# Kernel optimization log

Measured on AMD Instinct MI355X. Metric: run time of the kernel, lower is better.

Reference implementation:

```python
import jax, jax.numpy as jnp
import numpy as np

D_MODEL = 1024
N_HEADS = 16
D_K = D_MODEL // N_HEADS
B, L = 2, 2048


def setup_inputs() -> dict:
    key = jax.random.key(0)
    ks = jax.random.split(key, 13)
    s = 0.02
    inp = {
        'query': jax.random.normal(ks[0], (B, L, D_MODEL), jnp.float32),
        'key': jax.random.normal(ks[1], (B, L, D_MODEL), jnp.float32),
        'value': jax.random.normal(ks[2], (B, L, D_MODEL), jnp.float32),
        'mask': jax.random.randint(ks[3], (1, 1, L, L), 0, 2).astype(bool),
        'W_q': jax.random.normal(ks[4], (D_MODEL, D_MODEL), jnp.float32) * s,
        'b_q': jnp.zeros((D_MODEL,), jnp.float32),
        'W_k': jax.random.normal(ks[5], (D_MODEL, D_MODEL), jnp.float32) * s,
        'b_k': jnp.zeros((D_MODEL,), jnp.float32),
        'W_v': jax.random.normal(ks[6], (D_MODEL, D_MODEL), jnp.float32) * s,
        'b_v': jnp.zeros((D_MODEL,), jnp.float32),
        'W_o': jax.random.normal(ks[7], (D_MODEL, D_MODEL), jnp.float32) * s,
        'b_o': jnp.zeros((D_MODEL,), jnp.float32),
    }
    return inp


def _split_heads(x):
    b, l, _ = x.shape
    return x.reshape(b, l, N_HEADS, D_K).transpose(0, 2, 1, 3)  # [B,H,L,dk]


def reference(query, key, value, mask, W_q, b_q, W_k, b_k, W_v, b_v, W_o, b_o):
    q = _split_heads(query @ W_q + b_q)
    k = _split_heads(key @ W_k + b_k)
    v = _split_heads(value @ W_v + b_v)
    # Unscaled attention logits [B,H,L,L] (NO 1/sqrt(dk))
    logits = jnp.einsum('bhqd,bhkd->bhqk', q, k)
    logits = jnp.where(mask, -jnp.inf, logits)
    w = jax.nn.softmax(logits, axis=-1)
    w = jnp.nan_to_num(w, nan=0.0)  # fully-masked rows -> zeros
    attended = jnp.einsum('bhqk,bhkd->bhqd', w, v)
    # dropout in eval mode = identity; combine heads
    out = attended.transpose(0, 2, 1, 3).reshape(B, L, D_MODEL)
    return out @ W_o + b_o
```

## Files before the change

kernel.cpp:

```cpp
#include <hip/hip_runtime.h>
#include <hip/hip_bf16.h>
#include <stdint.h>


typedef __bf16 bf16;
typedef __bf16 bf16x8 __attribute__((ext_vector_type(8)));
typedef float f32x4 __attribute__((ext_vector_type(4)));

#define AS1 __attribute__((address_space(1)))
#define AS3 __attribute__((address_space(3)))

__device__ __forceinline__ void g2l16(const void* g, void* l) {
    __builtin_amdgcn_global_load_lds((AS1 void*)g, (AS3 void*)l, 16, 0, 0);
}

__device__ __forceinline__ bool lane_masked(unsigned long long m) {
#if __has_builtin(__builtin_amdgcn_inverse_ballot_w64)
    return __builtin_amdgcn_inverse_ballot_w64(m);
#else
    return (m >> (threadIdx.x & 63)) & 1ull;
#endif
}

#define LOG2E 1.44269504088896f

__global__ __launch_bounds__(256) void cvt3_kernel(const float* __restrict__ a0,
                                                   const float* __restrict__ a1,
                                                   const float* __restrict__ a2,
                                                   bf16* o0, bf16* o1, bf16* o2) {
    int y = blockIdx.y;
    const float* in = (y == 0) ? a0 : (y == 1) ? a1 : a2;
    bf16* out = (y == 0) ? o0 : (y == 1) ? o1 : o2;
    int idx = blockIdx.x * 256 + threadIdx.x;
    float4 v = ((const float4*)in)[idx];
    __align__(8) bf16 o[4];
    o[0] = (bf16)v.x; o[1] = (bf16)v.y; o[2] = (bf16)v.z; o[3] = (bf16)v.w;
    *(uint2*)(out + (size_t)idx * 4) = *(const uint2*)o;
}

__global__ __launch_bounds__(256) void mdetect_kernel(const unsigned int* __restrict__ w,
                                                      int* __restrict__ flag) {
    int idx = blockIdx.x * 256 + threadIdx.x;
    unsigned v = w[idx];
    int f = 0;
    if (v == 0x3F800000u) f = 2;
    else if (v > 1u) f = 1;
    unsigned long long b1 = __ballot(f & 1);
    unsigned long long b2 = __ballot(f & 2);
    if ((threadIdx.x & 63) == 0) {
        int agg = (b1 ? 1 : 0) | (b2 ? 2 : 0);
        if (agg) atomicOr(flag, agg);
    }
}

__global__ __launch_bounds__(256) void mpack_kernel(const void* __restrict__ mask,
                                                    unsigned long long* __restrict__ mb,
                                                    const int* __restrict__ flag) {
    int idx = blockIdx.x * 256 + threadIdx.x;
    int f = *flag;
    bool v;
    if (f & 2)      v = ((const float*)mask)[idx] != 0.0f;
    else if (f & 1) v = ((const unsigned char*)mask)[idx] != 0;
    else            v = ((const int*)mask)[idx] != 0;
    unsigned long long b = __ballot(v);
    if ((threadIdx.x & 63) == 0) mb[idx >> 6] = b;
}

__global__ __launch_bounds__(256) void rpack_kernel(const unsigned long long* __restrict__ mb,
                                                    unsigned long long* __restrict__ rmb) {
    int task = blockIdx.x * 4 + (threadIdx.x >> 6);
    int qg = task >> 5, kt = task & 31;
    int lane = threadIdx.x & 63, quad = lane >> 4, col = lane & 15;
    #pragma unroll
    for (int r = 0; r < 4; ++r) {
        unsigned long long wrow = mb[(size_t)(qg * 16 + quad * 4 + r) * 32 + kt];
        #pragma unroll
        for (int nt = 0; nt < 4; ++nt) {
            unsigned long long b = __ballot(((wrow >> (nt * 16 + col)) & 1ull) != 0);
            if (lane == 0) rmb[(size_t)task * 16 + r * 4 + nt] = b;
        }
    }
}

__global__ __launch_bounds__(256) void wtrans_kernel(const float* W0, const float* W1,
                                                     const float* W2, const float* W3,
                                                     bf16* T0, bf16* T1, bf16* T2, bf16* T3) {
    const float* W; bf16* T;
    int y = blockIdx.y;
    if (y == 0)      { W = W0; T = T0; }
    else if (y == 1) { W = W1; T = T1; }
    else if (y == 2) { W = W2; T = T2; }
    else             { W = W3; T = T3; }
    int tx = blockIdx.x & 15, ty = blockIdx.x >> 4;
    int n0 = tx * 64, k0 = ty * 64;
    __shared__ __align__(16) bf16 t[64 * 72];
    int tid = threadIdx.x;
    #pragma unroll
    for (int rr = 0; rr < 4; ++rr) {
        int idx = rr * 256 + tid;
        int r = idx >> 4, c4 = (idx & 15) * 4;
        float4 v = *(const float4*)(W + (size_t)(k0 + r) * 1024 + n0 + c4);
        __align__(8) bf16 o[4];
        o[0] = (bf16)v.x; o[1] = (bf16)v.y; o[2] = (bf16)v.z; o[3] = (bf16)v.w;
        *(uint2*)&t[r * 72 + c4] = *(const uint2*)o;
    }
    __syncthreads();
    #pragma unroll
    for (int rr = 0; rr < 2; ++rr) {
        int idx = rr * 256 + tid;
        int n = idx >> 3, kc = (idx & 7) * 8;
        __align__(16) bf16 o[8];
        #pragma unroll
        for (int j = 0; j < 8; ++j) o[j] = t[(kc + j) * 72 + n];
        *(uint4*)(T + (size_t)(n0 + n) * 1024 + k0 + kc) = *(const uint4*)o;
    }
}

template <int MODE>
__device__ __forceinline__ void gemm128_core(const bf16* __restrict__ A,
                                             const bf16* __restrict__ Bt,
                                             const float* __restrict__ bias,
                                             void* __restrict__ Out, int bm, int bn,
                                             float scale) {
    __shared__ __align__(16) bf16 la[128 * 32];
    __shared__ __align__(16) bf16 lb[128 * 32];
    int tid = threadIdx.x;
    int w = tid >> 6, lane = tid & 63;
    int quad = lane >> 4, col = lane & 15;
    int wm = w >> 1, wn = w & 1;
    int m0 = bm * 128, n0 = bn * 128;
    f32x4 acc[4][4];
    f32x4 z = {0.f, 0.f, 0.f, 0.f};
    #pragma unroll
    for (int i = 0; i < 4; ++i)
        #pragma unroll
        for (int j = 0; j < 4; ++j) acc[i][j] = z;
    int srow = lane >> 2;
    int skc = (lane & 3) * 8;
    for (int kt = 0; kt < 32; ++kt) {
        int kk = kt * 32;
        __syncthreads();
        #pragma unroll
        for (int rr = 0; rr < 2; ++rr) {
            int ch = rr * 4 + w;
            int row = ch * 16 + srow;
            g2l16(A + (size_t)(m0 + row) * 1024 + kk + skc, &la[ch * 512]);
            g2l16(Bt + (size_t)(n0 + row) * 1024 + kk + skc, &lb[ch * 512]);
        }
        __syncthreads();
        bf16x8 af[4], bfr[4];
        #pragma unroll
        for (int mt = 0; mt < 4; ++mt)
            af[mt] = *(const bf16x8*)&la[(wm * 64 + mt * 16 + col) * 32 + quad * 8];
        #pragma unroll
        for (int nt = 0; nt < 4; ++nt)
            bfr[nt] = *(const bf16x8*)&lb[(wn * 64 + nt * 16 + col) * 32 + quad * 8];
        #pragma unroll
        for (int mt = 0; mt < 4; ++mt)
            #pragma unroll
            for (int nt = 0; nt < 4; ++nt)
                acc[mt][nt] = __builtin_amdgcn_mfma_f32_16x16x32_bf16(
                    af[mt], bfr[nt], acc[mt][nt], 0, 0, 0);
    }
    float bia[4];
    #pragma unroll
    for (int nt = 0; nt < 4; ++nt) bia[nt] = bias[n0 + wn * 64 + nt * 16 + col];
    #pragma unroll
    for (int mt = 0; mt < 4; ++mt) {
        #pragma unroll
        for (int nt = 0; nt < 4; ++nt) {
            #pragma unroll
            for (int r = 0; r < 4; ++r) {
                int m = m0 + wm * 64 + mt * 16 + quad * 4 + r;
                int n = n0 + wn * 64 + nt * 16 + col;
                float v = (acc[mt][nt][r] + bia[nt]) * scale;
                if (MODE == 0) {
                    int b = m >> 11, l = m & 2047, h = n >> 6, d = n & 63;
                    ((bf16*)Out)[(((size_t)b * 16 + h) * 2048 + l) * 64 + d] = (bf16)v;
                } else {
                    int b = m >> 11, l = m & 2047, h = n >> 6, d = n & 63;
                    ((bf16*)Out)[(((size_t)b * 16 + h) * 64 + d) * 2048 + l] = (bf16)v;
                }
            }
        }
    }
}

__global__ __launch_bounds__(256) void qkv_kernel(
    const bf16* Xq, const bf16* Xk, const bf16* Xv,
    const bf16* Wq, const bf16* Wk, const bf16* Wv,
    const float* bq, const float* bk, const float* bv,
    bf16* Qh, bf16* Kh, bf16* Vt) {
    int y = blockIdx.y;
    int bm = blockIdx.x >> 3, bn = blockIdx.x & 7;
    if (y == 0)      gemm128_core<0>(Xq, Wq, bq, Qh, bm, bn, LOG2E);
    else if (y == 1) gemm128_core<0>(Xk, Wk, bk, Kh, bm, bn, 1.0f);
    else             gemm128_core<2>(Xv, Wv, bv, Vt, bm, bn, 1.0f);
}

__global__ __launch_bounds__(256) void ogemm_kernel(const bf16* __restrict__ A,
                                                    const bf16* __restrict__ Wt,
                                                    const float* __restrict__ bias,
                                                    float* __restrict__ Out) {
    int bm = blockIdx.x >> 3, bn = blockIdx.x & 7;
    __shared__ __align__(16) bf16 la[64 * 32];
    __shared__ __align__(16) bf16 lb[128 * 32];
    int tid = threadIdx.x;
    int w = tid >> 6, lane = tid & 63;
    int quad = lane >> 4, col = lane & 15;
    int m0 = bm * 64, n0 = bn * 128;
    f32x4 acc[4][2];
    f32x4 z = {0.f, 0.f, 0.f, 0.f};
    #pragma unroll
    for (int i = 0; i < 4; ++i) { acc[i][0] = z; acc[i][1] = z; }
    int srow = lane >> 2;
    int skc = (lane & 3) * 8;
    for (int kt = 0; kt < 32; ++kt) {
        int kk = kt * 32;
        __syncthreads();
        g2l16(A + (size_t)(m0 + w * 16 + srow) * 1024 + kk + skc, &la[w * 512]);
        #pragma unroll
        for (int rr = 0; rr < 2; ++rr) {
            int ch = rr * 4 + w;
            g2l16(Wt + (size_t)(n0 + ch * 16 + srow) * 1024 + kk + skc, &lb[ch * 512]);
        }
        __syncthreads();
        bf16x8 af[4], bfr[2];
        #pragma unroll
        for (int mt = 0; mt < 4; ++mt)
            af[mt] = *(const bf16x8*)&la[(mt * 16 + col) * 32 + quad * 8];
        #pragma unroll
        for (int nt = 0; nt < 2; ++nt)
            bfr[nt] = *(const bf16x8*)&lb[(w * 32 + nt * 16 + col) * 32 + quad * 8];
        #pragma unroll
        for (int mt = 0; mt < 4; ++mt)
            #pragma unroll
            for (int nt = 0; nt < 2; ++nt)
                acc[mt][nt] = __builtin_amdgcn_mfma_f32_16x16x32_bf16(
                    af[mt], bfr[nt], acc[mt][nt], 0, 0, 0);
    }
    float bia[2];
    bia[0] = bias[n0 + w * 32 + col];
    bia[1] = bias[n0 + w * 32 + 16 + col];
    #pragma unroll
    for (int mt = 0; mt < 4; ++mt)
        #pragma unroll
        for (int nt = 0; nt < 2; ++nt)
            #pragma unroll
            for (int r = 0; r < 4; ++r)
                Out[(size_t)(m0 + mt * 16 + quad * 4 + r) * 1024 +
                    n0 + w * 32 + nt * 16 + col] = acc[mt][nt][r] + bia[nt];
}

__global__ __launch_bounds__(128) void attn_kernel(const bf16* __restrict__ Qh,
                                                   const bf16* __restrict__ Kh,
                                                   const bf16* __restrict__ Vt,
                                                   const unsigned long long* __restrict__ rmb,
                                                   bf16* __restrict__ att) {
    int bh = blockIdx.x, qt = blockIdx.y;
    int b = bh >> 4, h = bh & 15;
    int q0 = qt * 64;
    __shared__ __align__(16) bf16 ks[64 * 64];
    __shared__ __align__(16) bf16 vs[64 * 64];
    __shared__ __align__(16) bf16 ps[2 * 32 * 72];
    int tid = threadIdx.x;
    int w = tid >> 6, lane = tid & 63;
    int quad = lane >> 4, col = lane & 15;
    int c7 = col & 7;
    int sr = lane >> 3;
    int sg = (lane & 7) ^ sr;
    int swz0 = (quad ^ c7) * 8;
    int swz1 = ((4 + quad) ^ c7) * 8;

    int mofs = __builtin_amdgcn_readfirstlane((qt * 4 + w * 2) * 512);

    #pragma unroll
    for (int i = 0; i < 4; ++i) {
        int ch = w * 4 + i;
        g2l16(Qh + ((size_t)bh * 2048 + q0 + ch * 8 + sr) * 64 + sg * 8, &ks[ch * 512]);
    }
    __syncthreads();
    bf16x8 aq[2][2];
    #pragma unroll
    for (int mt = 0; mt < 2; ++mt) {
        aq[mt][0] = *(const bf16x8*)&ks[(w * 32 + mt * 16 + col) * 64 + swz0];
        aq[mt][1] = *(const bf16x8*)&ks[(w * 32 + mt * 16 + col) * 64 + swz1];
    }
    bf16x8 onesf;
    #pragma unroll
    for (int i = 0; i < 8; ++i) onesf[i] = (bf16)1.0f;

    f32x4 z = {0.f, 0.f, 0.f, 0.f};
    f32x4 O[2][4], R[2];
    #pragma unroll
    for (int mt = 0; mt < 2; ++mt) {
        R[mt] = z;
        #pragma unroll
        for (int i = 0; i < 4; ++i) O[mt][i] = z;
    }

    for (int kt = 0; kt < 32; ++kt) {
        __syncthreads();
        #pragma unroll
        for (int i = 0; i < 4; ++i) {
            int ch = w * 4 + i;
            int r = ch * 8 + sr;
            g2l16(Kh + ((size_t)bh * 2048 + kt * 64 + r) * 64 + sg * 8, &ks[ch * 512]);
            g2l16(Vt + ((size_t)bh * 64 + r) * 2048 + kt * 64 + sg * 8, &vs[ch * 512]);
        }
        __syncthreads();

        f32x4 s[2][4];
        #pragma unroll
        for (int nt = 0; nt < 4; ++nt) {
            s[0][nt] = z; s[1][nt] = z;
            bf16x8 bk0 = *(const bf16x8*)&ks[(nt * 16 + col) * 64 + swz0];
            s[0][nt] = __builtin_amdgcn_mfma_f32_16x16x32_bf16(aq[0][0], bk0, s[0][nt], 0, 0, 0);
            s[1][nt] = __builtin_amdgcn_mfma_f32_16x16x32_bf16(aq[1][0], bk0, s[1][nt], 0, 0, 0);
            bf16x8 bk1 = *(const bf16x8*)&ks[(nt * 16 + col) * 64 + swz1];
            s[0][nt] = __builtin_amdgcn_mfma_f32_16x16x32_bf16(aq[0][1], bk1, s[0][nt], 0, 0, 0);
            s[1][nt] = __builtin_amdgcn_mfma_f32_16x16x32_bf16(aq[1][1], bk1, s[1][nt], 0, 0, 0);
        }

        #pragma unroll
        for (int mt = 0; mt < 2; ++mt) {
            const unsigned long long* mw = rmb + mofs + mt * 512 + kt * 16;
            #pragma unroll
            for (int r = 0; r < 4; ++r) {
                #pragma unroll
                for (int nt = 0; nt < 4; ++nt) {
                    float p = __builtin_amdgcn_exp2f(s[mt][nt][r]);
                    if (lane_masked(mw[r * 4 + nt])) p = 0.0f;
                    ps[w * 2304 + (mt * 16 + quad * 4 + r) * 72 + nt * 16 + col] = (bf16)p;
                }
            }
        }

        bf16x8 ap[2][2];
        #pragma unroll
        for (int mt = 0; mt < 2; ++mt) {
            ap[mt][0] = *(const bf16x8*)&ps[w * 2304 + (mt * 16 + col) * 72 + quad * 8];
            ap[mt][1] = *(const bf16x8*)&ps[w * 2304 + (mt * 16 + col) * 72 + 32 + quad * 8];
        }
        #pragma unroll
        for (int dt = 0; dt < 4; ++dt) {
            bf16x8 bv0 = *(const bf16x8*)&vs[(dt * 16 + col) * 64 + swz0];
            O[0][dt] = __builtin_amdgcn_mfma_f32_16x16x32_bf16(ap[0][0], bv0, O[0][dt], 0, 0, 0);
            O[1][dt] = __builtin_amdgcn_mfma_f32_16x16x32_bf16(ap[1][0], bv0, O[1][dt], 0, 0, 0);
            bf16x8 bv1 = *(const bf16x8*)&vs[(dt * 16 + col) * 64 + swz1];
            O[0][dt] = __builtin_amdgcn_mfma_f32_16x16x32_bf16(ap[0][1], bv1, O[0][dt], 0, 0, 0);
            O[1][dt] = __builtin_amdgcn_mfma_f32_16x16x32_bf16(ap[1][1], bv1, O[1][dt], 0, 0, 0);
        }
        #pragma unroll
        for (int mt = 0; mt < 2; ++mt) {
            R[mt] = __builtin_amdgcn_mfma_f32_16x16x32_bf16(ap[mt][0], onesf, R[mt], 0, 0, 0);
            R[mt] = __builtin_amdgcn_mfma_f32_16x16x32_bf16(ap[mt][1], onesf, R[mt], 0, 0, 0);
        }
    }

    #pragma unroll
    for (int mt = 0; mt < 2; ++mt) {
        #pragma unroll
        for (int r = 0; r < 4; ++r) {
            float rsv = R[mt][r];
            float inv = (rsv > 0.f) ? 1.0f / rsv : 0.f;
            int qg = q0 + w * 32 + mt * 16 + quad * 4 + r;
            #pragma unroll
            for (int dt = 0; dt < 4; ++dt) {
                float ov = O[mt][dt][r] * inv;
                att[((size_t)b * 2048 + qg) * 1024 + h * 64 + dt * 16 + col] = (bf16)ov;
            }
        }
    }
}

extern "C" void kernel_launch(void* const* d_in, const int* in_sizes, int n_in,
                              void* d_out, int out_size, void* d_ws, size_t ws_size,
                              hipStream_t stream) {
    (void)in_sizes; (void)n_in; (void)out_size; (void)ws_size;
    const float* query = (const float*)d_in[0];
    const float* key_  = (const float*)d_in[1];
    const float* value = (const float*)d_in[2];
    const void*  mask  = d_in[3];
    const float* W_q = (const float*)d_in[4];
    const float* b_q = (const float*)d_in[5];
    const float* W_k = (const float*)d_in[6];
    const float* b_k = (const float*)d_in[7];
    const float* W_v = (const float*)d_in[8];
    const float* b_v = (const float*)d_in[9];
    const float* W_o = (const float*)d_in[10];
    const float* b_o = (const float*)d_in[11];

    char* ws = (char*)d_ws;
    bf16* Xq  = (bf16*)(ws + 0);
    bf16* Xk  = (bf16*)(ws + 8388608);
    bf16* Xv  = (bf16*)(ws + 16777216);
    bf16* Wtq = (bf16*)(ws + 25165824);
    bf16* Wtk = (bf16*)(ws + 27262976);
    bf16* Wtv = (bf16*)(ws + 29360128);
    bf16* Wto = (bf16*)(ws + 31457280);
    bf16* Qh  = (bf16*)(ws + 33554432);
    bf16* Kh  = (bf16*)(ws + 41943040);
    bf16* Vt  = (bf16*)(ws + 50331648);
    bf16* att = (bf16*)(ws + 58720256);
    unsigned long long* mb  = (unsigned long long*)(ws + 67108864);
    unsigned long long* rmb = (unsigned long long*)(ws + 67633152);
    int* flag = (int*)(ws + 68157440);

    hipMemsetAsync(flag, 0, 4, stream);
    mdetect_kernel<<<4096, 256, 0, stream>>>((const unsigned int*)mask, flag);
    mpack_kernel<<<16384, 256, 0, stream>>>(mask, mb, flag);
    rpack_kernel<<<1024, 256, 0, stream>>>(mb, rmb);

    cvt3_kernel<<<dim3(4096, 3), 256, 0, stream>>>(query, key_, value, Xq, Xk, Xv);
    wtrans_kernel<<<dim3(256, 4), 256, 0, stream>>>(W_q, W_k, W_v, W_o, Wtq, Wtk, Wtv, Wto);

    qkv_kernel<<<dim3(256, 3), 256, 0, stream>>>(Xq, Xk, Xv, Wtq, Wtk, Wtv,
                                                 b_q, b_k, b_v, Qh, Kh, Vt);
    attn_kernel<<<dim3(32, 32), 128, 0, stream>>>(Qh, Kh, Vt, rmb, att);
    ogemm_kernel<<<512, 256, 0, stream>>>(att, Wto, b_o, (float*)d_out);
}
```

Baseline: 271.8 us.

## Fuse activation fp32->bf16 conversion into QKV GEMM and merge mask prep kernels

Removes the separate cvt3 kernel so the QKV GEMM loads fp32 activations directly, converts them in registers and stores bf16 into LDS. The mask detect/pack/repack chain becomes a single-wavefront detect kernel that samples only the first 4096 words, plus a packing path folded into the weight-transpose kernel. This cuts several launches and the intermediate bf16 and bitmask buffers. In exchange, A-tile loads in the GEMM become synchronous register loads instead of global_load_lds. The mask-type detection now looks at a sample rather than the whole mask, which could misclassify some masks.

```diff
diff --git a/kernel.cpp b/kernel.cpp
--- a/kernel.cpp
+++ b/kernel.cpp
@@ -24,69 +24,50 @@
 
 #define LOG2E 1.44269504088896f
 
-__global__ __launch_bounds__(256) void cvt3_kernel(const float* __restrict__ a0,
-                                                   const float* __restrict__ a1,
-                                                   const float* __restrict__ a2,
-                                                   bf16* o0, bf16* o1, bf16* o2) {
-    int y = blockIdx.y;
-    const float* in = (y == 0) ? a0 : (y == 1) ? a1 : a2;
-    bf16* out = (y == 0) ? o0 : (y == 1) ? o1 : o2;
-    int idx = blockIdx.x * 256 + threadIdx.x;
-    float4 v = ((const float4*)in)[idx];
-    __align__(8) bf16 o[4];
-    o[0] = (bf16)v.x; o[1] = (bf16)v.y; o[2] = (bf16)v.z; o[3] = (bf16)v.w;
-    *(uint2*)(out + (size_t)idx * 4) = *(const uint2*)o;
-}
-
-__global__ __launch_bounds__(256) void mdetect_kernel(const unsigned int* __restrict__ w,
-                                                      int* __restrict__ flag) {
-    int idx = blockIdx.x * 256 + threadIdx.x;
-    unsigned v = w[idx];
+__global__ __launch_bounds__(64) void mdetect_kernel(const unsigned int* __restrict__ w,
+                                                     int* __restrict__ flag) {
+    int lane = threadIdx.x;
     int f = 0;
-    if (v == 0x3F800000u) f = 2;
-    else if (v > 1u) f = 1;
+    #pragma unroll
+    for (int i = 0; i < 64; ++i) {
+        unsigned v = w[i * 64 + lane];
+        if (v == 0x3F800000u) f |= 2;
+        else if (v > 1u) f |= 1;
+    }
     unsigned long long b1 = __ballot(f & 1);
     unsigned long long b2 = __ballot(f & 2);
-    if ((threadIdx.x & 63) == 0) {
-        int agg = (b1 ? 1 : 0) | (b2 ? 2 : 0);
-        if (agg) atomicOr(flag, agg);
-    }
-}
-
-__global__ __launch_bounds__(256) void mpack_kernel(const void* __restrict__ mask,
-                                                    unsigned long long* __restrict__ mb,
-                                                    const int* __restrict__ flag) {
-    int idx = blockIdx.x * 256 + threadIdx.x;
-    int f = *flag;
-    bool v;
-    if (f & 2)      v = ((const float*)mask)[idx] != 0.0f;
-    else if (f & 1) v = ((const unsigned char*)mask)[idx] != 0;
-    else            v = ((const int*)mask)[idx] != 0;
-    unsigned long long b = __ballot(v);
-    if ((threadIdx.x & 63) == 0) mb[idx >> 6] = b;
-}
-
-__global__ __launch_bounds__(256) void rpack_kernel(const unsigned long long* __restrict__ mb,
-                                                    unsigned long long* __restrict__ rmb) {
-    int task = blockIdx.x * 4 + (threadIdx.x >> 6);
-    int qg = task >> 5, kt = task & 31;
-    int lane = threadIdx.x & 63, quad = lane >> 4, col = lane & 15;
-    #pragma unroll
-    for (int r = 0; r < 4; ++r) {
-        unsigned long long wrow = mb[(size_t)(qg * 16 + quad * 4 + r) * 32 + kt];
-        #pragma unroll
-        for (int nt = 0; nt < 4; ++nt) {
-            unsigned long long b = __ballot(((wrow >> (nt * 16 + col)) & 1ull) != 0);
-            if (lane == 0) rmb[(size_t)task * 16 + r * 4 + nt] = b;
-        }
-    }
-}
-
-__global__ __launch_bounds__(256) void wtrans_kernel(const float* W0, const float* W1,
-                                                     const float* W2, const float* W3,
-                                                     bf16* T0, bf16* T1, bf16* T2, bf16* T3) {
+    if (lane == 0) flag[0] = b2 ? 2 : (b1 ? 1 : 0);
+}
+
+__global__ __launch_bounds__(256) void prep_kernel(
+    const float* W0, const float* W1, const float* W2, const float* W3,
+    bf16* T0, bf16* T1, bf16* T2, bf16* T3,
+    const void* __restrict__ mask, const int* __restrict__ flag,
+    unsigned long long* __restrict__ rmb) {
+    int y = blockIdx.y;
+    int tid = threadIdx.x;
+    if (y >= 4) {
+        int task = ((y - 4) * 256 + blockIdx.x) * 4 + (tid >> 6);
+        int qg = task >> 5, kt = task & 31;
+        int lane = tid & 63, quad = lane >> 4, col = lane & 15;
+        int f = *flag;
+        #pragma unroll
+        for (int r = 0; r < 4; ++r) {
+            int row = qg * 16 + quad * 4 + r;
+            #pragma unroll
+            for (int nt = 0; nt < 4; ++nt) {
+                size_t e = (size_t)row * 2048 + kt * 64 + nt * 16 + col;
+                bool v;
+                if (f & 2)      v = ((const float*)mask)[e] != 0.0f;
+                else if (f & 1) v = ((const unsigned char*)mask)[e] != 0;
+                else            v = ((const int*)mask)[e] != 0;
+                unsigned long long b = __ballot(v);
+                if (lane == 0) rmb[(size_t)task * 16 + r * 4 + nt] = b;
+            }
+        }
+        return;
+    }
     const float* W; bf16* T;
-    int y = blockIdx.y;
     if (y == 0)      { W = W0; T = T0; }
     else if (y == 1) { W = W1; T = T1; }
     else if (y == 2) { W = W2; T = T2; }
@@ -94,7 +75,6 @@
     int tx = blockIdx.x & 15, ty = blockIdx.x >> 4;
     int n0 = tx * 64, k0 = ty * 64;
     __shared__ __align__(16) bf16 t[64 * 72];
-    int tid = threadIdx.x;
     #pragma unroll
     for (int rr = 0; rr < 4; ++rr) {
         int idx = rr * 256 + tid;
@@ -117,7 +97,7 @@
 }
 
 template <int MODE>
-__device__ __forceinline__ void gemm128_core(const bf16* __restrict__ A,
+__device__ __forceinline__ void gemm128_core(const float* __restrict__ A,
                                              const bf16* __restrict__ Bt,
                                              const float* __restrict__ bias,
                                              void* __restrict__ Out, int bm, int bn,
@@ -144,7 +124,13 @@
         for (int rr = 0; rr < 2; ++rr) {
             int ch = rr * 4 + w;
             int row = ch * 16 + srow;
-            g2l16(A + (size_t)(m0 + row) * 1024 + kk + skc, &la[ch * 512]);
+            const float* ap_ = A + (size_t)(m0 + row) * 1024 + kk + skc;
+            float4 v0 = *(const float4*)ap_;
+            float4 v1 = *(const float4*)(ap_ + 4);
+            __align__(16) bf16 o[8];
+            o[0] = (bf16)v0.x; o[1] = (bf16)v0.y; o[2] = (bf16)v0.z; o[3] = (bf16)v0.w;
+            o[4] = (bf16)v1.x; o[5] = (bf16)v1.y; o[6] = (bf16)v1.z; o[7] = (bf16)v1.w;
+            *(uint4*)&la[ch * 512 + lane * 8] = *(const uint4*)o;
             g2l16(Bt + (size_t)(n0 + row) * 1024 + kk + skc, &lb[ch * 512]);
         }
         __syncthreads();
@@ -187,7 +173,7 @@
 }
 
 __global__ __launch_bounds__(256) void qkv_kernel(
-    const bf16* Xq, const bf16* Xk, const bf16* Xv,
+    const float* Xq, const float* Xk, const float* Xv,
     const bf16* Wq, const bf16* Wk, const bf16* Wv,
     const float* bq, const float* bk, const float* bv,
     bf16* Qh, bf16* Kh, bf16* Vt) {
@@ -392,30 +378,22 @@
     const float* b_o = (const float*)d_in[11];
 
     char* ws = (char*)d_ws;
-    bf16* Xq  = (bf16*)(ws + 0);
-    bf16* Xk  = (bf16*)(ws + 8388608);
-    bf16* Xv  = (bf16*)(ws + 16777216);
+    bf16* Qh  = (bf16*)(ws + 0);
+    bf16* Kh  = (bf16*)(ws + 8388608);
+    bf16* Vt  = (bf16*)(ws + 16777216);
     bf16* Wtq = (bf16*)(ws + 25165824);
     bf16* Wtk = (bf16*)(ws + 27262976);
     bf16* Wtv = (bf16*)(ws + 29360128);
     bf16* Wto = (bf16*)(ws + 31457280);
-    bf16* Qh  = (bf16*)(ws + 33554432);
-    bf16* Kh  = (bf16*)(ws + 41943040);
-    bf16* Vt  = (bf16*)(ws + 50331648);
-    bf16* att = (bf16*)(ws + 58720256);
-    unsigned long long* mb  = (unsigned long long*)(ws + 67108864);
-    unsigned long long* rmb = (unsigned long long*)(ws + 67633152);
-    int* flag = (int*)(ws + 68157440);
-
-    hipMemsetAsync(flag, 0, 4, stream);
-    mdetect_kernel<<<4096, 256, 0, stream>>>((const unsigned int*)mask, flag);
-    mpack_kernel<<<16384, 256, 0, stream>>>(mask, mb, flag);
-    rpack_kernel<<<1024, 256, 0, stream>>>(mb, rmb);
-
-    cvt3_kernel<<<dim3(4096, 3), 256, 0, stream>>>(query, key_, value, Xq, Xk, Xv);
-    wtrans_kernel<<<dim3(256, 4), 256, 0, stream>>>(W_q, W_k, W_v, W_o, Wtq, Wtk, Wtv, Wto);
-
-    qkv_kernel<<<dim3(256, 3), 256, 0, stream>>>(Xq, Xk, Xv, Wtq, Wtk, Wtv,
+    bf16* att = (bf16*)(ws + 33554432);
+    unsigned long long* rmb = (unsigned long long*)(ws + 50331648);
+    int* flag = (int*)(ws + 50855936);
+
+    mdetect_kernel<<<1, 64, 0, stream>>>((const unsigned int*)mask, flag);
+    prep_kernel<<<dim3(256, 8), 256, 0, stream>>>(W_q, W_k, W_v, W_o,
+                                                  Wtq, Wtk, Wtv, Wto,
+                                                  mask, flag, rmb);
+    qkv_kernel<<<dim3(256, 3), 256, 0, stream>>>(query, key_, value, Wtq, Wtk, Wtv,
                                                  b_q, b_k, b_v, Qh, Kh, Vt);
     attn_kernel<<<dim3(32, 32), 128, 0, stream>>>(Qh, Kh, Vt, rmb, att);
     ogemm_kernel<<<512, 256, 0, stream>>>(att, Wto, b_o, (float*)d_out);
```

Result: no change. 276.8 us (+1.8%).
